# Performance work log

Hardware: AMD Instinct MI355X
Metric: run time of the kernel (lower is better)

Reference implementation:

```python
import jax, jax.numpy as jnp
import numpy as np

S = 2048
HIDDEN = 4096
NH, NKV, HD = 32, 8, 128
QPK = NH // NKV  # 4
BLOCK, LOCAL, VERT = 64, 16, 8
ROPE_BASE = 1.0e6
SCALE = 1.0 / HD  # mup scaling: head_dim / mup_attn_multiplier(=1.0)


def setup_inputs() -> dict:
    key = jax.random.key(0)
    ks = jax.random.split(key, 5)
    qkv_out = NKV * (QPK + 2) * HD  # 6144, head-major layout
    return {
        "positions": jnp.arange(S, dtype=jnp.int32),
        "hidden_states": jax.random.normal(ks[0], (S, HIDDEN), jnp.float32),
        "w_qkv": jax.random.normal(ks[1], (qkv_out, HIDDEN), jnp.float32) * 0.02,
        "b_qkv": jax.random.normal(ks[2], (qkv_out,), jnp.float32) * 0.02,
        "w_dense": jax.random.normal(ks[3], (HIDDEN, HIDDEN), jnp.float32) * 0.02,
        "b_dense": jax.random.normal(ks[4], (HIDDEN,), jnp.float32) * 0.02,
    }


def _rope(x, cos, sin):
    # NeoX-style (non-interleaved) rotary over full head_dim.
    # x: [S, n_heads, HD]; cos/sin: [S, HD//2]
    d2 = x.shape[-1] // 2
    x1, x2 = x[..., :d2], x[..., d2:]
    c, s = cos[:, None, :], sin[:, None, :]
    return jnp.concatenate([x1 * c - x2 * s, x2 * c + x1 * s], axis=-1)


def _blocksparse_mask(positions):
    # vllm phi3small pattern: block (qb,kb) active iff causal AND
    # (qb-kb < local_blocks OR (kb + head + 1) % vert_stride == 0), hetero heads.
    qb = positions // BLOCK                       # [S]
    heads = jnp.arange(NH, dtype=positions.dtype)
    diff = qb[:, None] - qb[None, :]              # [S,S]
    local = diff < LOCAL                          # [S,S]
    vert = ((qb[None, None, :] + heads[:, None, None] + 1) % VERT) == 0  # [NH,1,S]
    causal = positions[:, None] >= positions[None, :]                     # [S,S]
    return (local[None] | vert) & causal[None]    # [NH,S,S]


def reference(positions, hidden_states, w_qkv, b_qkv, w_dense, b_dense):
    seq = hidden_states.shape[0]
    qkv = hidden_states @ w_qkv.T + b_qkv                   # [S, 6144]
    qkv = qkv.reshape(seq, NKV, QPK + 2, HD)                # head-major split
    q = qkv[:, :, :QPK].reshape(seq, NH, HD)
    k = qkv[:, :, QPK]                                      # [S, NKV, HD]
    v = qkv[:, :, QPK + 1]

    pos = positions.astype(jnp.float32)  # rope_position_scale = 1.0
    inv_freq = 1.0 / (ROPE_BASE ** (jnp.arange(0, HD, 2, dtype=jnp.float32) / HD))
    freqs = pos[:, None] * inv_freq                          # [S, HD/2]
    cos, sin = jnp.cos(freqs), jnp.sin(freqs)
    q = _rope(q, cos, sin)
    k = _rope(k, cos, sin)

    # GQA: each kv head serves QPK query heads
    kx = jnp.repeat(k, QPK, axis=1)                          # [S, NH, HD]
    vx = jnp.repeat(v, QPK, axis=1)

    scores = jnp.einsum('qhd,khd->hqk', q, kx) * SCALE       # [NH,S,S]
    mask = _blocksparse_mask(positions)
    scores = jnp.where(mask, scores, -jnp.inf)  # diag always in local block -> no empty rows
    p = jax.nn.softmax(scores, axis=-1)
    out = jnp.einsum('hqk,khd->qhd', p, vx).reshape(seq, NH * HD)
    return out @ w_dense.T + b_dense
```

## Files before the change

### kernel.cpp

```cpp
#include <hip/hip_runtime.h>

#define S_LEN   2048
#define HID     4096
#define NHEADS  32
#define NKVH    8
#define HDIM    128
#define NQKV    6144
#define ATT_SCALE (1.0f/128.0f)

typedef unsigned short u16;
typedef __attribute__((ext_vector_type(8))) __bf16 bf16x8;
typedef __attribute__((ext_vector_type(4))) float  f32x4;

__device__ __forceinline__ u16 f2bf(float f) {
    union { float f; unsigned u; } x; x.f = f;
    unsigned u = x.u;
    u += 0x7fffu + ((u >> 16) & 1u);
    return (u16)(u >> 16);
}
__device__ __forceinline__ float bf2f(u16 v) {
    union { unsigned u; float f; } x; x.u = ((unsigned)v) << 16; return x.f;
}

__global__ __launch_bounds__(256) void cvt_bf16_kernel(const float* __restrict__ in,
                                                       u16* __restrict__ out, int n4) {
    int stride = gridDim.x * blockDim.x;
    for (int i = blockIdx.x * blockDim.x + threadIdx.x; i < n4; i += stride) {
        float4 v = *(const float4*)(in + (size_t)i * 4);
        ushort4 o = make_ushort4(f2bf(v.x), f2bf(v.y), f2bf(v.z), f2bf(v.w));
        *(ushort4*)(out + (size_t)i * 4) = o;
    }
}

#define GFENCE() asm volatile("" ::: "memory")
#define GSBAR()  do { GFENCE(); __builtin_amdgcn_s_barrier(); GFENCE(); } while (0)

template <int BN_, int NB_, bool OUT_BF16>
__global__ __launch_bounds__(512, 2) void gemm_fc_kernel(
    const u16* __restrict__ A,
    const u16* __restrict__ B,
    const float* __restrict__ bias,
    void* __restrict__ Cout,
    int M, int N, int K)
{
    constexpr int LB = BN_ / 128;
    constexpr int VM = 2 + LB;
    __shared__ u16 lds[16384 + 2 * BN_ * 64];

    const int tid  = threadIdx.x;
    const int wid  = tid >> 6;
    const int lane = tid & 63;
    const int ln   = lane & 15;
    const int quad = lane >> 4;
    const int wr   = wid >> 2;
    const int wc   = wid & 3;
    const int tileM = blockIdx.y * 128;
    const int tileN = blockIdx.x * BN_;

    f32x4 acc[2][NB_][4];
    #pragma unroll
    for (int b = 0; b < 2; b++)
        #pragma unroll
        for (int n = 0; n < NB_; n++)
            #pragma unroll
            for (int m = 0; m < 4; m++) {
                f32x4 z = {0.f, 0.f, 0.f, 0.f};
                acc[b][n][m] = z;
            }

    const int srho = lane >> 3;
    const int scol = (((lane & 7) ^ srho) << 3);

    auto gload = [&](const u16* src, u16* dst) {
        __builtin_amdgcn_global_load_lds(
            (const __attribute__((address_space(1))) void*)src,
            (__attribute__((address_space(3))) void*)dst, 16, 0, 0);
    };
    auto stage_A = [&](int kk, int bb) {
        const int base = bb * 8192;
        #pragma unroll
        for (int s = 0; s < 2; s++) {
            const int rho0 = s * 64 + wid * 8;
            const int rho  = rho0 + srho;
            const u16* src = A + (size_t)(tileM + rho) * K + (size_t)kk * 64 + scol;
            gload(src, &lds[base + rho0 * 64]);
        }
    };
    auto stage_Bh = [&](int h, int kk, int bb) {
        const int base = 16384 + bb * (BN_ * 64) + h * ((BN_ / 2) * 64);
        #pragma unroll
        for (int s = 0; s < LB; s++) {
            const int rho0 = s * 64 + wid * 8;
            const int rho  = rho0 + srho;
            const u16* src = B + (size_t)(tileN + h * (BN_ / 2) + rho) * K
                               + (size_t)kk * 64 + scol;
            gload(src, &lds[base + rho0 * 64]);
        }
    };

#define WAIT_VM()                                                                   \
    do {                                                                            \
        if constexpr (VM == 5) asm volatile("s_waitcnt vmcnt(5)" ::: "memory");     \
        else                   asm volatile("s_waitcnt vmcnt(4)" ::: "memory");     \
    } while (0)

#define READ_A()                                                                    \
    do {                                                                            \
        _Pragma("unroll")                                                           \
        for (int m = 0; m < 4; m++) {                                               \
            const int ra = wr * 64 + m * 16 + ln;                                   \
            const int ab = buf * 8192 + ra * 64;                                    \
            const int rx = ra & 7;                                                  \
            af[m][0] = *(const bf16x8*)(&lds[ab + ((quad ^ rx) << 3)]);             \
            af[m][1] = *(const bf16x8*)(&lds[ab + (((4 + quad) ^ rx) << 3)]);       \
        }                                                                           \
    } while (0)

#define MFMA_B(b_)                                                                  \
    do {                                                                            \
        __builtin_amdgcn_s_setprio(1);                                              \
        _Pragma("unroll")                                                           \
        for (int n = 0; n < NB_; n++) {                                             \
            const int rb = (b_) * (BN_ / 2) + wc * (NB_ * 16) + n * 16 + ln;        \
            const int bb = 16384 + buf * (BN_ * 64) + rb * 64;                      \
            const int rx = rb & 7;                                                  \
            bf16x8 b0 = *(const bf16x8*)(&lds[bb + ((quad ^ rx) << 3)]);            \
            bf16x8 b1 = *(const bf16x8*)(&lds[bb + (((4 + quad) ^ rx) << 3)]);      \
            _Pragma("unroll")                                                       \
            for (int m = 0; m < 4; m++) {                                           \
                acc[b_][n][m] = __builtin_amdgcn_mfma_f32_16x16x32_bf16(            \
                    af[m][0], b0, acc[b_][n][m], 0, 0, 0);                          \
                acc[b_][n][m] = __builtin_amdgcn_mfma_f32_16x16x32_bf16(            \
                    af[m][1], b1, acc[b_][n][m], 0, 0, 0);                          \
            }                                                                       \
        }                                                                           \
        __builtin_amdgcn_s_setprio(0);                                              \
    } while (0)

    const int nIter = K / 64;

    stage_A(0, 0); stage_Bh(0, 0, 0); stage_Bh(1, 0, 0);

    bf16x8 af[4][2];

    for (int t = 0; t < nIter; t++) {
        const int buf = t & 1;
        const int bn  = buf ^ 1;
        const int kn  = (t + 1 == nIter) ? 0 : t + 1;

        stage_A(kn, bn);
        WAIT_VM();
        GSBAR();
        READ_A();
        MFMA_B(0);

        stage_Bh(0, kn, bn);
        WAIT_VM();
        GSBAR();
        MFMA_B(1);
        stage_Bh(1, kn, bn);

        asm volatile("s_waitcnt lgkmcnt(0)" ::: "memory");
        GSBAR();
    }

    asm volatile("s_waitcnt vmcnt(0)" ::: "memory");

#undef WAIT_VM
#undef READ_A
#undef MFMA_B

    #pragma unroll
    for (int b = 0; b < 2; b++)
        #pragma unroll
        for (int n = 0; n < NB_; n++) {
            const int col = tileN + b * (BN_ / 2) + wc * (NB_ * 16) + n * 16 + ln;
            const float bv = bias[col];
            #pragma unroll
            for (int m = 0; m < 4; m++) {
                #pragma unroll
                for (int r = 0; r < 4; r++) {
                    const int row = tileM + wr * 64 + m * 16 + quad * 4 + r;
                    float v = acc[b][n][m][r] + bv;
                    if (OUT_BF16)
                        ((u16*)Cout)[(size_t)row * N + col] = f2bf(v);
                    else
                        ((float*)Cout)[(size_t)row * N + col] = v;
                }
            }
        }
}

__global__ __launch_bounds__(256) void rope_cs_kernel(
    const int* __restrict__ positions, float2* __restrict__ cs)
{
    int i = blockIdx.x * 256 + threadIdx.x;
    if (i >= S_LEN * 64) return;
    int pos = i >> 6, d2 = i & 63;
    float p = (float)positions[pos];
    float inv = expf(-(float)d2 * (13.815510557964274f / 64.0f));
    float s, c;
    sincosf(p * inv, &s, &c);
    cs[i] = make_float2(c, s);
}

__global__ __launch_bounds__(64) void rope_split_kernel(
    const u16* __restrict__ qkv, const float2* __restrict__ cs,
    u16* __restrict__ qb_o, u16* __restrict__ kb_o)
{
    const int pos  = blockIdx.x;
    const int t    = threadIdx.x;
    const int hy   = blockIdx.y * 8 + (t >> 3);
    const int d2_0 = (t & 7) * 8;

    const u16* src;
    u16* dst;
    if (hy < NHEADS) {
        int kv = hy >> 2, qi = hy & 3;
        src = qkv + (size_t)pos * NQKV + (kv * 6 + qi) * HDIM;
        dst = qb_o + ((size_t)hy * S_LEN + pos) * HDIM;
    } else {
        int kv = hy - NHEADS;
        src = qkv + (size_t)pos * NQKV + (kv * 6 + 4) * HDIM;
        dst = kb_o + ((size_t)kv * S_LEN + pos) * HDIM;
    }

    uint4 v1 = *(const uint4*)(src + d2_0);
    uint4 v2 = *(const uint4*)(src + d2_0 + 64);
    const u16* p1 = (const u16*)&v1;
    const u16* p2 = (const u16*)&v2;
    const float2* csr = cs + pos * 64 + d2_0;

    u16 o1[8], o2[8];
    #pragma unroll
    for (int j = 0; j < 8; j++) {
        float c = csr[j].x, s = csr[j].y;
        float x1 = bf2f(p1[j]), x2 = bf2f(p2[j]);
        o1[j] = f2bf(x1 * c - x2 * s);
        o2[j] = f2bf(x2 * c + x1 * s);
    }
    *(uint4*)(dst + d2_0)      = *(uint4*)o1;
    *(uint4*)(dst + d2_0 + 64) = *(uint4*)o2;
}

__global__ __launch_bounds__(256) void vtrans_kernel(
    const u16* __restrict__ qkv,
    u16* __restrict__ VT)
{
    __shared__ u16 T[64][HDIM + 8];
    const int s0 = blockIdx.x * 64;
    const int kv = blockIdx.y;
    const int tid = threadIdx.x;
    #pragma unroll
    for (int p = 0; p < 4; p++) {
        int pos = p * 16 + (tid >> 4);
        int d   = (tid & 15) * 8;
        *(uint4*)&T[pos][d] =
            *(const uint4*)(qkv + (size_t)(s0 + pos) * NQKV + (kv * 6 + 5) * HDIM + d);
    }
    __syncthreads();
    #pragma unroll
    for (int p = 0; p < 4; p++) {
        int d  = p * 32 + (tid >> 3);
        int sc = (tid & 7) * 8;
        u16 tmp[8];
        #pragma unroll
        for (int j = 0; j < 8; j++) tmp[j] = T[sc + j][d];
        *(uint4*)(VT + ((size_t)kv * HDIM + d) * S_LEN + s0 + sc) = *(uint4*)tmp;
    }
}

__global__ __launch_bounds__(512, 4) void attn_bs_kernel(
    const u16* __restrict__ Q,
    const u16* __restrict__ K,
    const u16* __restrict__ V,
    u16* __restrict__ O)
{
    __shared__ u16 Ks[64 * 128];
    __shared__ u16 Vt[128 * 64];
    __shared__ u16 Ps[8][16 * 64];

    const int blk = (int)gridDim.x - 1 - (int)blockIdx.x;
    const int h   = blockIdx.y;
    const int kv  = h >> 2;
    const int tid  = threadIdx.x;
    const int w    = tid >> 6;
    const int lane = tid & 63;
    const int ln   = lane & 15;
    const int quad = lane >> 4;
    const int qbw  = 2 * blk + (w >> 2);
    const int rb16 = (w & 3) * 16;

    bf16x8 aq[4];
    {
        const u16* Qg = Q + ((size_t)h * S_LEN + qbw * 64 + rb16 + ln) * HDIM + quad * 8;
        #pragma unroll
        for (int ks = 0; ks < 4; ks++)
            aq[ks] = *(const bf16x8*)(Qg + ks * 32);
    }

    f32x4 oacc[8];
    #pragma unroll
    for (int n = 0; n < 8; n++) { f32x4 z = {0.f,0.f,0.f,0.f}; oacc[n] = z; }
    float mrow[4] = {-1e30f, -1e30f, -1e30f, -1e30f};
    float lrow[4] = {0.f, 0.f, 0.f, 0.f};

    const int kbMax = 2 * blk + 1;
    for (int kb = 0; kb <= kbMax; kb++) {
        const bool vert = (((kb + h + 1) & 7) == 0);
        const bool selu = ((kbMax - kb) < 17) || vert;
        if (!selu) continue;

        __syncthreads();

        const u16* Kg  = K + ((size_t)kv * S_LEN + kb * 64) * HDIM;
        const u16* VTg = V + (size_t)kv * HDIM * S_LEN + kb * 64;

        #pragma unroll
        for (int p = 0; p < 2; p++) {
            int r0  = w * 8 + p * 4;
            int row = r0 + (lane >> 4);
            const u16* src = Kg + (size_t)row * HDIM + (((lane & 15) ^ (row & 7)) << 3);
            __builtin_amdgcn_global_load_lds(
                (const __attribute__((address_space(1))) void*)src,
                (__attribute__((address_space(3))) void*)&Ks[r0 * 128], 16, 0, 0);
        }
        #pragma unroll
        for (int p = 0; p < 2; p++) {
            int r0  = w * 16 + p * 8;
            int row = r0 + (lane >> 3);
            int c   = (lane & 7) ^ (row & 7);
            const u16* src = VTg + (size_t)row * S_LEN + c * 8;
            __builtin_amdgcn_global_load_lds(
                (const __attribute__((address_space(1))) void*)src,
                (__attribute__((address_space(3))) void*)&Vt[r0 * 64], 16, 0, 0);
        }
        __syncthreads();

        const bool mine = (kb <= qbw) && (((qbw - kb) < 16) || vert);
        if (mine) {
            f32x4 sacc[4];
            #pragma unroll
            for (int jj = 0; jj < 4; jj++) { f32x4 z = {0.f,0.f,0.f,0.f}; sacc[jj] = z; }
            __builtin_amdgcn_s_setprio(1);
            #pragma unroll
            for (int ks = 0; ks < 4; ks++) {
                #pragma unroll
                for (int jj = 0; jj < 4; jj++) {
                    bf16x8 bk = *(const bf16x8*)(
                        &Ks[(jj * 16 + ln) * 128 + (((ks * 4 + quad) ^ (ln & 7)) << 3)]);
                    sacc[jj] = __builtin_amdgcn_mfma_f32_16x16x32_bf16(aq[ks], bk, sacc[jj], 0, 0, 0);
                }
            }
            __builtin_amdgcn_s_setprio(0);

            const bool diag = (kb == qbw);
            float pv[4][4], mxr[4];
            bool grow = false;
            #pragma unroll
            for (int r = 0; r < 4; r++) {
                const int qrow = rb16 + quad * 4 + r;
                float mx = -1e30f;
                #pragma unroll
                for (int jj = 0; jj < 4; jj++) {
                    float s = sacc[jj][r] * ATT_SCALE;
                    if (diag && (jj * 16 + ln) > qrow) s = -1e30f;
                    pv[r][jj] = s;
                    mx = fmaxf(mx, s);
                }
                #pragma unroll
                for (int off = 1; off < 16; off <<= 1)
                    mx = fmaxf(mx, __shfl_xor(mx, off, 64));
                mxr[r] = mx;
                grow |= (mx > mrow[r] + 8.0f);
            }
            if (__any(grow)) {
                #pragma unroll
                for (int r = 0; r < 4; r++) {
                    float mnew  = fmaxf(mrow[r], mxr[r]);
                    float alpha = __expf(mrow[r] - mnew);
                    lrow[r] *= alpha;
                    mrow[r]  = mnew;
                    #pragma unroll
                    for (int n = 0; n < 8; n++) oacc[n][r] *= alpha;
                }
            }
            #pragma unroll
            for (int r = 0; r < 4; r++) {
                float sum = 0.f;
                #pragma unroll
                for (int jj = 0; jj < 4; jj++) {
                    float pe = __expf(pv[r][jj] - mrow[r]);
                    pv[r][jj] = pe;
                    sum += pe;
                }
                #pragma unroll
                for (int off = 1; off < 16; off <<= 1)
                    sum += __shfl_xor(sum, off, 64);
                lrow[r] += sum;
                const int prow = quad * 4 + r;
                #pragma unroll
                for (int jj = 0; jj < 4; jj++)
                    Ps[w][prow * 64 + (((jj * 2 + (ln >> 3)) ^ (prow & 7)) << 3) + (ln & 7)]
                        = f2bf(pv[r][jj]);
            }

            __builtin_amdgcn_s_setprio(1);
            #pragma unroll
            for (int kk = 0; kk < 2; kk++) {
                bf16x8 ap = *(const bf16x8*)(
                    &Ps[w][ln * 64 + (((kk * 4 + quad) ^ (ln & 7)) << 3)]);
                #pragma unroll
                for (int n = 0; n < 8; n++) {
                    bf16x8 bv = *(const bf16x8*)(
                        &Vt[(n * 16 + ln) * 64 + (((kk * 4 + quad) ^ (ln & 7)) << 3)]);
                    oacc[n] = __builtin_amdgcn_mfma_f32_16x16x32_bf16(ap, bv, oacc[n], 0, 0, 0);
                }
            }
            __builtin_amdgcn_s_setprio(0);
        }
    }

    #pragma unroll
    for (int n = 0; n < 8; n++) {
        #pragma unroll
        for (int r = 0; r < 4; r++) {
            int pos = qbw * 64 + rb16 + quad * 4 + r;
            float o = oacc[n][r] / lrow[r];
            O[(size_t)pos * (NHEADS * HDIM) + h * HDIM + n * 16 + ln] = f2bf(o);
        }
    }
}

extern "C" void kernel_launch(void* const* d_in, const int* in_sizes, int n_in,
                              void* d_out, int out_size, void* d_ws, size_t ws_size,
                              hipStream_t stream) {
    const int*   positions = (const int*)d_in[0];
    const float* hidden    = (const float*)d_in[1];
    const float* w_qkv     = (const float*)d_in[2];
    const float* b_qkv     = (const float*)d_in[3];
    const float* w_dense   = (const float*)d_in[4];
    const float* b_dense   = (const float*)d_in[5];
    float* out = (float*)d_out;

    char* ws = (char*)d_ws;
    u16* ws_h    = (u16*)(ws);
    u16* ws_wqkv = (u16*)(ws + 16777216);
    u16* ws_wd   = (u16*)(ws + 67108864);
    u16* ws_qkv  = (u16*)(ws + 100663296);
    u16* ws_q    = (u16*)(ws + 125829120);
    u16* ws_k    = (u16*)(ws + 142606336);
    u16* ws_v    = (u16*)(ws + 146800640);
    u16* ws_attn = (u16*)(ws + 150994944);
    float2* ws_cs = (float2*)(ws + 150994944);

    cvt_bf16_kernel<<<1024, 256, 0, stream>>>(hidden,  ws_h,    (S_LEN * HID) / 4);
    cvt_bf16_kernel<<<2048, 256, 0, stream>>>(w_qkv,   ws_wqkv, (NQKV * HID) / 4);
    cvt_bf16_kernel<<<2048, 256, 0, stream>>>(w_dense, ws_wd,   (HID * HID) / 4);

    gemm_fc_kernel<384, 3, true><<<dim3(NQKV / 384, S_LEN / 128), 512, 0, stream>>>(
        ws_h, ws_wqkv, b_qkv, ws_qkv, S_LEN, NQKV, HID);

    rope_cs_kernel<<<(S_LEN * 64) / 256, 256, 0, stream>>>(positions, ws_cs);
    rope_split_kernel<<<dim3(S_LEN, 5), 64, 0, stream>>>(ws_qkv, ws_cs, ws_q, ws_k);

    vtrans_kernel<<<dim3(S_LEN / 64, NKVH), 256, 0, stream>>>(ws_qkv, ws_v);

    attn_bs_kernel<<<dim3(S_LEN / 128, NHEADS), 512, 0, stream>>>(ws_q, ws_k, ws_v, ws_attn);

    gemm_fc_kernel<256, 2, false><<<dim3(HID / 256, S_LEN / 128), 512, 0, stream>>>(
        ws_attn, ws_wd, b_dense, out, S_LEN, HID, HID);
}
```

Before: 489.7 us.

## Fuse Q rotary into attention prologue and merge weight conversion launches

Query RoPE is now applied inside the attention kernel, which reads Q directly from the packed QKV buffer and rotates it in registers. This removes the separate Q write and re-read through a standalone rope pass, leaving a rope kernel that handles only K. The three fp32-to-bf16 conversion launches are also merged into one kernel, which saves launch overhead but adds per-element branching. The Q loads from the packed layout are strided by NQKV per row and may coalesce less well than the old head-contiguous buffer.

```diff
diff --git a/kernel.cpp b/kernel.cpp
--- a/kernel.cpp
+++ b/kernel.cpp
@@ -22,13 +22,21 @@
     union { unsigned u; float f; } x; x.u = ((unsigned)v) << 16; return x.f;
 }
 
-__global__ __launch_bounds__(256) void cvt_bf16_kernel(const float* __restrict__ in,
-                                                       u16* __restrict__ out, int n4) {
+__global__ __launch_bounds__(256) void cvt3_kernel(
+    const float* __restrict__ in0, u16* __restrict__ out0, int n0,
+    const float* __restrict__ in1, u16* __restrict__ out1, int n1,
+    const float* __restrict__ in2, u16* __restrict__ out2, int n2)
+{
     int stride = gridDim.x * blockDim.x;
-    for (int i = blockIdx.x * blockDim.x + threadIdx.x; i < n4; i += stride) {
-        float4 v = *(const float4*)(in + (size_t)i * 4);
+    int total = n0 + n1 + n2;
+    for (int i = blockIdx.x * blockDim.x + threadIdx.x; i < total; i += stride) {
+        const float* in; u16* out; int j;
+        if (i < n0)           { in = in0; out = out0; j = i; }
+        else if (i < n0 + n1) { in = in1; out = out1; j = i - n0; }
+        else                  { in = in2; out = out2; j = i - n0 - n1; }
+        float4 v = *(const float4*)(in + (size_t)j * 4);
         ushort4 o = make_ushort4(f2bf(v.x), f2bf(v.y), f2bf(v.z), f2bf(v.w));
-        *(ushort4*)(out + (size_t)i * 4) = o;
+        *(ushort4*)(out + (size_t)j * 4) = o;
     }
 }
 
@@ -204,26 +212,17 @@
     cs[i] = make_float2(c, s);
 }
 
-__global__ __launch_bounds__(64) void rope_split_kernel(
+__global__ __launch_bounds__(64) void rope_k_kernel(
     const u16* __restrict__ qkv, const float2* __restrict__ cs,
-    u16* __restrict__ qb_o, u16* __restrict__ kb_o)
+    u16* __restrict__ kb_o)
 {
     const int pos  = blockIdx.x;
     const int t    = threadIdx.x;
-    const int hy   = blockIdx.y * 8 + (t >> 3);
+    const int kv   = t >> 3;
     const int d2_0 = (t & 7) * 8;
 
-    const u16* src;
-    u16* dst;
-    if (hy < NHEADS) {
-        int kv = hy >> 2, qi = hy & 3;
-        src = qkv + (size_t)pos * NQKV + (kv * 6 + qi) * HDIM;
-        dst = qb_o + ((size_t)hy * S_LEN + pos) * HDIM;
-    } else {
-        int kv = hy - NHEADS;
-        src = qkv + (size_t)pos * NQKV + (kv * 6 + 4) * HDIM;
-        dst = kb_o + ((size_t)kv * S_LEN + pos) * HDIM;
-    }
+    const u16* src = qkv + (size_t)pos * NQKV + (kv * 6 + 4) * HDIM;
+    u16* dst       = kb_o + ((size_t)kv * S_LEN + pos) * HDIM;
 
     uint4 v1 = *(const uint4*)(src + d2_0);
     uint4 v2 = *(const uint4*)(src + d2_0 + 64);
@@ -231,7 +230,9 @@
     const u16* p2 = (const u16*)&v2;
     const float2* csr = cs + pos * 64 + d2_0;
 
-    u16 o1[8], o2[8];
+    uint4 w1, w2;
+    u16* o1 = (u16*)&w1;
+    u16* o2 = (u16*)&w2;
     #pragma unroll
     for (int j = 0; j < 8; j++) {
         float c = csr[j].x, s = csr[j].y;
@@ -239,8 +240,8 @@
         o1[j] = f2bf(x1 * c - x2 * s);
         o2[j] = f2bf(x2 * c + x1 * s);
     }
-    *(uint4*)(dst + d2_0)      = *(uint4*)o1;
-    *(uint4*)(dst + d2_0 + 64) = *(uint4*)o2;
+    *(uint4*)(dst + d2_0)      = w1;
+    *(uint4*)(dst + d2_0 + 64) = w2;
 }
 
 __global__ __launch_bounds__(256) void vtrans_kernel(
@@ -263,15 +264,17 @@
     for (int p = 0; p < 4; p++) {
         int d  = p * 32 + (tid >> 3);
         int sc = (tid & 7) * 8;
-        u16 tmp[8];
+        uint4 wv;
+        u16* tmp = (u16*)&wv;
         #pragma unroll
         for (int j = 0; j < 8; j++) tmp[j] = T[sc + j][d];
-        *(uint4*)(VT + ((size_t)kv * HDIM + d) * S_LEN + s0 + sc) = *(uint4*)tmp;
+        *(uint4*)(VT + ((size_t)kv * HDIM + d) * S_LEN + s0 + sc) = wv;
     }
 }
 
 __global__ __launch_bounds__(512, 4) void attn_bs_kernel(
-    const u16* __restrict__ Q,
+    const u16* __restrict__ qkv,
+    const float2* __restrict__ cs,
     const u16* __restrict__ K,
     const u16* __restrict__ V,
     u16* __restrict__ O)
@@ -293,10 +296,30 @@
 
     bf16x8 aq[4];
     {
-        const u16* Qg = Q + ((size_t)h * S_LEN + qbw * 64 + rb16 + ln) * HDIM + quad * 8;
+        const int pos = qbw * 64 + rb16 + ln;
+        const int qi  = h & 3;
+        const u16* Qg = qkv + (size_t)pos * NQKV + (kv * 6 + qi) * HDIM + quad * 8;
+        uint4 raw[4], rq[4];
         #pragma unroll
         for (int ks = 0; ks < 4; ks++)
-            aq[ks] = *(const bf16x8*)(Qg + ks * 32);
+            raw[ks] = *(const uint4*)(Qg + ks * 32);
+        const u16* pp = (const u16*)raw;
+        u16* rp = (u16*)rq;
+        const float2* csr = cs + pos * 64 + quad * 8;
+        #pragma unroll
+        for (int g = 0; g < 2; g++) {
+            #pragma unroll
+            for (int j = 0; j < 8; j++) {
+                float2 cv = csr[g * 32 + j];
+                float x1 = bf2f(pp[g * 8 + j]);
+                float x2 = bf2f(pp[(g + 2) * 8 + j]);
+                rp[g * 8 + j]       = f2bf(x1 * cv.x - x2 * cv.y);
+                rp[(g + 2) * 8 + j] = f2bf(x2 * cv.x + x1 * cv.y);
+            }
+        }
+        #pragma unroll
+        for (int ks = 0; ks < 4; ks++)
+            aq[ks] = *(const bf16x8*)&rq[ks];
     }
 
     f32x4 oacc[8];
@@ -448,25 +471,26 @@
     u16* ws_wqkv = (u16*)(ws + 16777216);
     u16* ws_wd   = (u16*)(ws + 67108864);
     u16* ws_qkv  = (u16*)(ws + 100663296);
-    u16* ws_q    = (u16*)(ws + 125829120);
+    float2* ws_cs = (float2*)(ws + 125829120);
     u16* ws_k    = (u16*)(ws + 142606336);
     u16* ws_v    = (u16*)(ws + 146800640);
     u16* ws_attn = (u16*)(ws + 150994944);
-    float2* ws_cs = (float2*)(ws + 150994944);
-
-    cvt_bf16_kernel<<<1024, 256, 0, stream>>>(hidden,  ws_h,    (S_LEN * HID) / 4);
-    cvt_bf16_kernel<<<2048, 256, 0, stream>>>(w_qkv,   ws_wqkv, (NQKV * HID) / 4);
-    cvt_bf16_kernel<<<2048, 256, 0, stream>>>(w_dense, ws_wd,   (HID * HID) / 4);
+
+    cvt3_kernel<<<4096, 256, 0, stream>>>(
+        hidden,  ws_h,    (S_LEN * HID) / 4,
+        w_qkv,   ws_wqkv, (NQKV * HID) / 4,
+        w_dense, ws_wd,   (HID * HID) / 4);
 
     gemm_fc_kernel<384, 3, true><<<dim3(NQKV / 384, S_LEN / 128), 512, 0, stream>>>(
         ws_h, ws_wqkv, b_qkv, ws_qkv, S_LEN, NQKV, HID);
 
     rope_cs_kernel<<<(S_LEN * 64) / 256, 256, 0, stream>>>(positions, ws_cs);
-    rope_split_kernel<<<dim3(S_LEN, 5), 64, 0, stream>>>(ws_qkv, ws_cs, ws_q, ws_k);
+    rope_k_kernel<<<S_LEN, 64, 0, stream>>>(ws_qkv, ws_cs, ws_k);
 
     vtrans_kernel<<<dim3(S_LEN / 64, NKVH), 256, 0, stream>>>(ws_qkv, ws_v);
 
-    attn_bs_kernel<<<dim3(S_LEN / 128, NHEADS), 512, 0, stream>>>(ws_q, ws_k, ws_v, ws_attn);
+    attn_bs_kernel<<<dim3(S_LEN / 128, NHEADS), 512, 0, stream>>>(
+        ws_qkv, ws_cs, ws_k, ws_v, ws_attn);
 
     gemm_fc_kernel<256, 2, false><<<dim3(HID / 256, S_LEN / 128), 512, 0, stream>>>(
         ws_attn, ws_wd, b_dense, out, S_LEN, HID, HID);
```

Result: no change. 499.4 us (+2.0%).
